# Kernel optimization log

Hardware: AMD Instinct MI355X
Metric: run time of the kernel (lower is better)

The kernel has to match this reference:

```python
import jax, jax.numpy as jnp
import numpy as np

N = 4096  # seq len, used for cos/sin positional reweighting


def _non_neg(x):
    # exp(x) for x<0, x+1 for x>=0
    return jnp.where(x < 0, jnp.exp(x), x + 1.0)


def setup_inputs() -> dict:
    key = jax.random.key(0)
    kq, kk, kv = jax.random.split(key, 3)
    shape = (4, 16, N, 64)
    q = jax.random.normal(kq, shape, dtype=jnp.float32)
    k = jax.random.normal(kk, shape, dtype=jnp.float32)
    v = jax.random.normal(kv, shape, dtype=jnp.float32)
    return {"q": q, "k": k, "v": v}


def reference(q, k, v):
    s = q.shape[-2]
    pos = (jnp.pi / 2.0 / s) * jnp.arange(s, dtype=q.dtype)
    cos = jnp.cos(pos)[:, None]  # [S, 1], broadcasts over feature dim
    sin = jnp.sin(pos)[:, None]
    qf = _non_neg(q)
    kf = _non_neg(k)
    q_cos, q_sin = qf * cos, qf * sin  # [B, H, S, D]
    k_cos, k_sin = kf * cos, kf * sin
    # O(N) kv aggregation: [B, H, D, Dv]
    kv_cos = jnp.einsum('bhsd,bhse->bhde', k_cos, v)
    kv_sin = jnp.einsum('bhsd,bhse->bhde', k_sin, v)
    out = jnp.einsum('bhsd,bhde->bhse', q_cos, kv_cos) + \
          jnp.einsum('bhsd,bhde->bhse', q_sin, kv_sin)
    return out
```

## Files before the change

### kernel.cpp

```cpp
#include <hip/hip_runtime.h>
#include <math.h>

#define SLEN 4096
#define DH   64
#define BHN  64
#define CH   16
#define ROWSPER 256

typedef float  f32x4   __attribute__((ext_vector_type(4)));
typedef float  f32x16  __attribute__((ext_vector_type(16)));
typedef short  s16x4   __attribute__((ext_vector_type(4)));
typedef __bf16 bf16x8  __attribute__((ext_vector_type(8)));

static constexpr float ANG = 3.8349519697141029e-4f;

static __device__ __forceinline__ float featf(float x) {
    return x < 0.f ? __expf(x) : x + 1.f;
}
static __device__ __forceinline__ float b2f(short s) {
    unsigned u = ((unsigned)(unsigned short)s) << 16;
    float f; __builtin_memcpy(&f, &u, 4); return f;
}
static __device__ __forceinline__ short f2b(float f) {
    __bf16 h = (__bf16)f; short s; __builtin_memcpy(&s, &h, 2); return s;
}

__global__ __launch_bounds__(256) void kv_partial(const float* __restrict__ k,
                                                  const float* __restrict__ v,
                                                  short* __restrict__ part)
{
    static constexpr float CJ[8] = {
        1.0f, 0.999999926470f, 0.9999997058633f, 0.9999993381923f,
        0.9999988234532f, 0.9999981616455f, 0.9999973527695f, 0.9999963968250f};
    static constexpr float SJ[8] = {
        0.0f, 3.83495188e-4f, 7.66990319e-4f, 1.15048534e-3f,
        1.53398019e-3f, 1.91747481e-3f, 2.30096915e-3f, 2.68446316e-3f};
    static constexpr float RC16 = 0.99998117528260111f;
    static constexpr float RS16 = 6.1358846491544753e-3f;

    const int bx = blockIdx.x;
    const int bh = bx >> 4, ch = bx & 15;
    const size_t base = (size_t)bh * SLEN * DH;
    const int t  = threadIdx.x;
    const int w  = t >> 6;
    const int l  = t & 63;
    const int m  = l & 31;
    const int g  = l >> 5;
    const int dh = w >> 1;
    const int eh = w & 1;
    const int dcol = dh * 32 + m;
    const int ecol = eh * 32 + m;
    const int s_base = ch * ROWSPER;

    float c0, s0;
    __sincosf(ANG * (float)(s_base + g * 8), &s0, &c0);

    f32x16 accC = {}; f32x16 accS = {};
    float kr[2][8], vr[2][8];

#define LOADS(BUF, STEP) {                                                     \
        const size_t r0 = base + (size_t)(s_base + (STEP) * 16 + g * 8) * DH;  \
        _Pragma("unroll")                                                      \
        for (int j = 0; j < 8; ++j) {                                          \
            kr[BUF][j] = k[r0 + (size_t)j * DH + dcol];                        \
            vr[BUF][j] = v[r0 + (size_t)j * DH + ecol];                        \
        } }

    LOADS(0, 0)
    #pragma unroll
    for (int step = 0; step < 16; ++step) {
        const int buf = step & 1;
        if (step + 1 < 16) LOADS(buf ^ 1, step + 1)
        union { bf16x8 v; __bf16 e[8]; } Ac, As, Bv;
        #pragma unroll
        for (int j = 0; j < 8; ++j) {
            const float kf = featf(kr[buf][j]);
            const float p  = kf * c0;
            const float q  = kf * s0;
            Ac.e[j] = (__bf16)(p * CJ[j] - q * SJ[j]);
            As.e[j] = (__bf16)(q * CJ[j] + p * SJ[j]);
            Bv.e[j] = (__bf16)vr[buf][j];
        }
        accC = __builtin_amdgcn_mfma_f32_32x32x16_bf16(Ac.v, Bv.v, accC, 0, 0, 0);
        accS = __builtin_amdgcn_mfma_f32_32x32x16_bf16(As.v, Bv.v, accS, 0, 0, 0);
        const float cn = c0 * RC16 - s0 * RS16;
        s0 = s0 * RC16 + c0 * RS16;
        c0 = cn;
    }
#undef LOADS

    const size_t pb = (size_t)bx * 8192;
    #pragma unroll
    for (int r = 0; r < 16; ++r) {
        const int drow = dh * 32 + (r & 3) + 8 * (r >> 2) + 4 * g;
        const size_t o = pb + (size_t)drow * 64 + ecol;
        part[o]        = f2b(accC[r]);
        part[o + 4096] = f2b(accS[r]);
    }
}

__global__ __launch_bounds__(256) void kv_reduce(const short* __restrict__ part,
                                                 short* __restrict__ kvT)
{
    const int bx = blockIdx.x;
    const int bh = bx >> 3, seg = bx & 7;
    const size_t pbase = (size_t)bh * CH * 8192;
    const int j0 = seg * 1024 + threadIdx.x * 4;
    float acc[4] = {};
    #pragma unroll
    for (int c = 0; c < CH; ++c) {
        const s16x4 sv = *(const s16x4*)&part[pbase + (size_t)c * 8192 + j0];
        #pragma unroll
        for (int i = 0; i < 4; ++i) acc[i] += b2f(sv[i]);
    }
    const int cs = j0 >> 12;
    const int d  = (j0 >> 6) & 63;
    const int e0 = j0 & 63;
    #pragma unroll
    for (int i = 0; i < 4; ++i)
        kvT[(size_t)bh * 8192 + cs * 4096 + (e0 + i) * 64 + d] = f2b(acc[i]);
}

__global__ __launch_bounds__(256) void out_kernel(const float* __restrict__ q,
                                                  const short* __restrict__ kvT,
                                                  float* __restrict__ out)
{
    const int bx = blockIdx.x;
    const int bh = bx >> 4, chunk = bx & 15;
    const int t = threadIdx.x;
    const int wv = t >> 6, ln = t & 63, m = ln & 15, g = ln >> 4;
    const size_t qbase = (size_t)bh * SLEN * DH;
    const size_t kvb   = (size_t)bh * 8192;

    bf16x8 Bc[4][2], Bs[4][2];
    #pragma unroll
    for (int nt = 0; nt < 4; ++nt)
        #pragma unroll
        for (int b = 0; b < 2; ++b) {
            const int off = (nt * 16 + m) * 64 + b * 32 + g * 8;
            Bc[nt][b] = *(const bf16x8*)&kvT[kvb + off];
            Bs[nt][b] = *(const bf16x8*)&kvT[kvb + 4096 + off];
        }

    const int sA = chunk * 256 + wv * 16 + m;
    f32x4 qb[4], qn[4];
    #pragma unroll
    for (int p = 0; p < 4; ++p)
        qb[p] = *(const f32x4*)&q[qbase + (size_t)sA * DH + (p >> 1) * 32 + g * 8 + (p & 1) * 4];

    for (int it = 0; it < 4; ++it) {
        const int srow = sA + it * 64;
        if (it < 3) {
            #pragma unroll
            for (int p = 0; p < 4; ++p)
                qn[p] = *(const f32x4*)&q[qbase + (size_t)(srow + 64) * DH + (p >> 1) * 32 + g * 8 + (p & 1) * 4];
        }
        float sn, c;
        __sincosf(ANG * (float)srow, &sn, &c);
        union { bf16x8 v; __bf16 e[8]; } Ac[2], As[2];
        #pragma unroll
        for (int p = 0; p < 4; ++p) {
            #pragma unroll
            for (int i = 0; i < 4; ++i) {
                const float qf = featf(qb[p][i]);
                Ac[p >> 1].e[(p & 1) * 4 + i] = (__bf16)(qf * c);
                As[p >> 1].e[(p & 1) * 4 + i] = (__bf16)(qf * sn);
            }
        }
        f32x4 acc[4] = {};
        #pragma unroll
        for (int nt = 0; nt < 4; ++nt) {
            acc[nt] = __builtin_amdgcn_mfma_f32_16x16x32_bf16(Ac[0].v, Bc[nt][0], acc[nt], 0, 0, 0);
            acc[nt] = __builtin_amdgcn_mfma_f32_16x16x32_bf16(Ac[1].v, Bc[nt][1], acc[nt], 0, 0, 0);
            acc[nt] = __builtin_amdgcn_mfma_f32_16x16x32_bf16(As[0].v, Bs[nt][0], acc[nt], 0, 0, 0);
            acc[nt] = __builtin_amdgcn_mfma_f32_16x16x32_bf16(As[1].v, Bs[nt][1], acc[nt], 0, 0, 0);
        }
        const int s0 = chunk * 256 + (it * 4 + wv) * 16;
        #pragma unroll
        for (int r = 0; r < 4; ++r) {
            const size_t ob = ((size_t)bh * SLEN + s0 + g * 4 + r) * 64;
            #pragma unroll
            for (int nt = 0; nt < 4; ++nt)
                out[ob + nt * 16 + m] = acc[nt][r];
        }
        if (it < 3) {
            #pragma unroll
            for (int p = 0; p < 4; ++p) qb[p] = qn[p];
        }
    }
}

extern "C" void kernel_launch(void* const* d_in, const int* in_sizes, int n_in,
                              void* d_out, int out_size, void* d_ws, size_t ws_size,
                              hipStream_t stream) {
    const float* q = (const float*)d_in[0];
    const float* k = (const float*)d_in[1];
    const float* v = (const float*)d_in[2];
    float* out  = (float*)d_out;
    short* part = (short*)d_ws;
    short* kvT  = (short*)((char*)d_ws + (size_t)BHN * CH * 8192 * 2);

    hipLaunchKernelGGL(kv_partial, dim3(BHN * CH), dim3(256), 0, stream, k, v, part);
    hipLaunchKernelGGL(kv_reduce,  dim3(BHN * 8),  dim3(256), 0, stream, part, kvT);
    hipLaunchKernelGGL(out_kernel, dim3(BHN * 16), dim3(256), 0, stream, q, kvT, out);
}
```

Before: 66.32 us.

## Restructure kv_partial into single-wave block with async global-to-LDS triple buffering

kv_partial shrinks from four waves to one wave per block, and that wave now computes all four 32x32 output quadrants. K and V tiles are streamed into LDS with global_load_lds in a three-buffer pipeline guarded by vmcnt waits. This replaces strided per-lane scalar global loads with coalesced 16-byte DMA, and each wave reuses its k features across two V halves. The cost is a quarter of the threads in flight per block, more accumulator registers (eight 16-wide accumulators) and a longer serial loop per wave, so latency hiding now depends on the software pipeline.

```diff
diff --git a/kernel.cpp b/kernel.cpp
--- a/kernel.cpp
+++ b/kernel.cpp
@@ -25,9 +25,13 @@
     __bf16 h = (__bf16)f; short s; __builtin_memcpy(&s, &h, 2); return s;
 }
 
-__global__ __launch_bounds__(256) void kv_partial(const float* __restrict__ k,
-                                                  const float* __restrict__ v,
-                                                  short* __restrict__ part)
+#define GLD(SRC, DST) __builtin_amdgcn_global_load_lds(                        \
+    (const __attribute__((address_space(1))) void*)(SRC),                      \
+    (__attribute__((address_space(3))) void*)(DST), 16, 0, 0)
+
+__global__ __launch_bounds__(64) void kv_partial(const float* __restrict__ k,
+                                                 const float* __restrict__ v,
+                                                 short* __restrict__ part)
 {
     static constexpr float CJ[8] = {
         1.0f, 0.999999926470f, 0.9999997058633f, 0.9999993381923f,
@@ -38,64 +42,97 @@
     static constexpr float RC16 = 0.99998117528260111f;
     static constexpr float RS16 = 6.1358846491544753e-3f;
 
+    __shared__ float kbuf[3][16][64];
+    __shared__ float vbuf[3][16][64];
+
     const int bx = blockIdx.x;
     const int bh = bx >> 4, ch = bx & 15;
     const size_t base = (size_t)bh * SLEN * DH;
-    const int t  = threadIdx.x;
-    const int w  = t >> 6;
-    const int l  = t & 63;
-    const int m  = l & 31;
-    const int g  = l >> 5;
-    const int dh = w >> 1;
-    const int eh = w & 1;
-    const int dcol = dh * 32 + m;
-    const int ecol = eh * 32 + m;
+    const int l = threadIdx.x;
+    const int m = l & 31;
+    const int g = l >> 5;
     const int s_base = ch * ROWSPER;
 
     float c0, s0;
     __sincosf(ANG * (float)(s_base + g * 8), &s0, &c0);
 
-    f32x16 accC = {}; f32x16 accS = {};
-    float kr[2][8], vr[2][8];
-
-#define LOADS(BUF, STEP) {                                                     \
-        const size_t r0 = base + (size_t)(s_base + (STEP) * 16 + g * 8) * DH;  \
+    f32x16 aC00 = {}, aC01 = {}, aC10 = {}, aC11 = {};
+    f32x16 aS00 = {}, aS01 = {}, aS10 = {}, aS11 = {};
+
+#define STAGE(TILE, BUF) do {                                                  \
+        const float* gk_ = k + base + (size_t)(s_base + (TILE) * 16) * DH + l * 4; \
+        const float* gv_ = v + base + (size_t)(s_base + (TILE) * 16) * DH + l * 4; \
         _Pragma("unroll")                                                      \
-        for (int j = 0; j < 8; ++j) {                                          \
-            kr[BUF][j] = k[r0 + (size_t)j * DH + dcol];                        \
-            vr[BUF][j] = v[r0 + (size_t)j * DH + ecol];                        \
-        } }
-
-    LOADS(0, 0)
-    #pragma unroll
-    for (int step = 0; step < 16; ++step) {
-        const int buf = step & 1;
-        if (step + 1 < 16) LOADS(buf ^ 1, step + 1)
-        union { bf16x8 v; __bf16 e[8]; } Ac, As, Bv;
+        for (int i_ = 0; i_ < 4; ++i_) {                                       \
+            GLD(gk_ + i_ * 256, &kbuf[BUF][i_ * 4][0]);                        \
+            GLD(gv_ + i_ * 256, &vbuf[BUF][i_ * 4][0]);                        \
+        } } while (0)
+
+    STAGE(0, 0);
+    STAGE(1, 1);
+
+    #pragma unroll
+    for (int t = 0; t < 16; ++t) {
+        const int buf = t % 3;
+        if (t == 15) { asm volatile("s_waitcnt vmcnt(0)" ::: "memory"); }
+        else         { asm volatile("s_waitcnt vmcnt(8)" ::: "memory"); }
+        __builtin_amdgcn_sched_barrier(0);
+
+        float k0[8], k1[8], v0[8], v1[8];
         #pragma unroll
         for (int j = 0; j < 8; ++j) {
-            const float kf = featf(kr[buf][j]);
-            const float p  = kf * c0;
-            const float q  = kf * s0;
-            Ac.e[j] = (__bf16)(p * CJ[j] - q * SJ[j]);
-            As.e[j] = (__bf16)(q * CJ[j] + p * SJ[j]);
-            Bv.e[j] = (__bf16)vr[buf][j];
-        }
-        accC = __builtin_amdgcn_mfma_f32_32x32x16_bf16(Ac.v, Bv.v, accC, 0, 0, 0);
-        accS = __builtin_amdgcn_mfma_f32_32x32x16_bf16(As.v, Bv.v, accS, 0, 0, 0);
+            k0[j] = kbuf[buf][g * 8 + j][m];
+            k1[j] = kbuf[buf][g * 8 + j][32 + m];
+            v0[j] = vbuf[buf][g * 8 + j][m];
+            v1[j] = vbuf[buf][g * 8 + j][32 + m];
+        }
+        __builtin_amdgcn_sched_barrier(0);
+        if (t + 2 < 16) STAGE(t + 2, (t + 2) % 3);
+        __builtin_amdgcn_sched_barrier(0);
+
+        union { bf16x8 v; __bf16 e[8]; } Ac0, Ac1, As0, As1, B0, B1;
+        #pragma unroll
+        for (int j = 0; j < 8; ++j) {
+            const float cj = c0 * CJ[j] - s0 * SJ[j];
+            const float sj = s0 * CJ[j] + c0 * SJ[j];
+            const float f0 = featf(k0[j]);
+            const float f1 = featf(k1[j]);
+            Ac0.e[j] = (__bf16)(f0 * cj);
+            As0.e[j] = (__bf16)(f0 * sj);
+            Ac1.e[j] = (__bf16)(f1 * cj);
+            As1.e[j] = (__bf16)(f1 * sj);
+            B0.e[j]  = (__bf16)v0[j];
+            B1.e[j]  = (__bf16)v1[j];
+        }
+        aC00 = __builtin_amdgcn_mfma_f32_32x32x16_bf16(Ac0.v, B0.v, aC00, 0, 0, 0);
+        aC01 = __builtin_amdgcn_mfma_f32_32x32x16_bf16(Ac0.v, B1.v, aC01, 0, 0, 0);
+        aC10 = __builtin_amdgcn_mfma_f32_32x32x16_bf16(Ac1.v, B0.v, aC10, 0, 0, 0);
+        aC11 = __builtin_amdgcn_mfma_f32_32x32x16_bf16(Ac1.v, B1.v, aC11, 0, 0, 0);
+        aS00 = __builtin_amdgcn_mfma_f32_32x32x16_bf16(As0.v, B0.v, aS00, 0, 0, 0);
+        aS01 = __builtin_amdgcn_mfma_f32_32x32x16_bf16(As0.v, B1.v, aS01, 0, 0, 0);
+        aS10 = __builtin_amdgcn_mfma_f32_32x32x16_bf16(As1.v, B0.v, aS10, 0, 0, 0);
+        aS11 = __builtin_amdgcn_mfma_f32_32x32x16_bf16(As1.v, B1.v, aS11, 0, 0, 0);
+
         const float cn = c0 * RC16 - s0 * RS16;
         s0 = s0 * RC16 + c0 * RS16;
         c0 = cn;
     }
-#undef LOADS
+#undef STAGE
 
     const size_t pb = (size_t)bx * 8192;
     #pragma unroll
     for (int r = 0; r < 16; ++r) {
-        const int drow = dh * 32 + (r & 3) + 8 * (r >> 2) + 4 * g;
-        const size_t o = pb + (size_t)drow * 64 + ecol;
-        part[o]        = f2b(accC[r]);
-        part[o + 4096] = f2b(accS[r]);
+        const int rb = (r & 3) + 8 * (r >> 2) + 4 * g;
+        const size_t o0 = pb + (size_t)rb * 64;
+        const size_t o1 = pb + (size_t)(32 + rb) * 64;
+        part[o0 + m]             = f2b(aC00[r]);
+        part[o0 + 32 + m]        = f2b(aC01[r]);
+        part[o1 + m]             = f2b(aC10[r]);
+        part[o1 + 32 + m]        = f2b(aC11[r]);
+        part[o0 + 4096 + m]      = f2b(aS00[r]);
+        part[o0 + 4096 + 32 + m] = f2b(aS01[r]);
+        part[o1 + 4096 + m]      = f2b(aS10[r]);
+        part[o1 + 4096 + 32 + m] = f2b(aS11[r]);
     }
 }
 
@@ -200,7 +237,7 @@
     short* part = (short*)d_ws;
     short* kvT  = (short*)((char*)d_ws + (size_t)BHN * CH * 8192 * 2);
 
-    hipLaunchKernelGGL(kv_partial, dim3(BHN * CH), dim3(256), 0, stream, k, v, part);
+    hipLaunchKernelGGL(kv_partial, dim3(BHN * CH), dim3(64),  0, stream, k, v, part);
     hipLaunchKernelGGL(kv_reduce,  dim3(BHN * 8),  dim3(256), 0, stream, part, kvT);
     hipLaunchKernelGGL(out_kernel, dim3(BHN * 16), dim3(256), 0, stream, q, kvT, out);
 }
```

Measured after the change: 69.18 us. 1.04x slower.

## Stage K/V tiles through LDS with async global_load_lds in a 4-deep pipeline

Applied to the files above, without the earlier changes.

The kv_partial kernel now loads each 16-row K/V tile with global_load_lds (16-byte direct-to-LDS loads) into a 4-slot shared ring, keeping three tiles in flight. Manual vmcnt waits and barriers order the stages. Threads then read their strided columns from LDS instead of issuing many scalar global loads, which is meant to improve coalescing and latency hiding. The price is extra LDS traffic, a block barrier every step, and sensitivity to the hand-counted vmcnt values. The rotation math was also reordered so the angle is computed per row before multiplying by the feature.

```diff
diff --git a/kernel.cpp b/kernel.cpp
--- a/kernel.cpp
+++ b/kernel.cpp
@@ -24,6 +24,10 @@
 static __device__ __forceinline__ short f2b(float f) {
     __bf16 h = (__bf16)f; short s; __builtin_memcpy(&s, &h, 2); return s;
 }
+
+#define GLD(SRC, DST) __builtin_amdgcn_global_load_lds(                        \
+    (const __attribute__((address_space(1))) void*)(SRC),                      \
+    (__attribute__((address_space(3))) void*)(DST), 16, 0, 0)
 
 __global__ __launch_bounds__(256) void kv_partial(const float* __restrict__ k,
                                                   const float* __restrict__ v,
@@ -38,62 +42,78 @@
     static constexpr float RC16 = 0.99998117528260111f;
     static constexpr float RS16 = 6.1358846491544753e-3f;
 
+    __shared__ float kbuf[4][16][64];
+    __shared__ float vbuf[4][16][64];
+
     const int bx = blockIdx.x;
     const int bh = bx >> 4, ch = bx & 15;
     const size_t base = (size_t)bh * SLEN * DH;
-    const int t  = threadIdx.x;
-    const int w  = t >> 6;
-    const int l  = t & 63;
+    const int tid = threadIdx.x;
+    const int w  = tid >> 6;
+    const int l  = tid & 63;
     const int m  = l & 31;
     const int g  = l >> 5;
     const int dh = w >> 1;
     const int eh = w & 1;
-    const int dcol = dh * 32 + m;
-    const int ecol = eh * 32 + m;
     const int s_base = ch * ROWSPER;
 
     float c0, s0;
     __sincosf(ANG * (float)(s_base + g * 8), &s0, &c0);
 
     f32x16 accC = {}; f32x16 accS = {};
-    float kr[2][8], vr[2][8];
-
-#define LOADS(BUF, STEP) {                                                     \
-        const size_t r0 = base + (size_t)(s_base + (STEP) * 16 + g * 8) * DH;  \
+
+#define STAGE(TILE, BUF) do {                                                  \
+        const size_t r_ = base + (size_t)(s_base + (TILE) * 16 + w * 4) * DH + l * 4; \
+        GLD(k + r_, &kbuf[BUF][w * 4][0]);                                     \
+        GLD(v + r_, &vbuf[BUF][w * 4][0]);                                     \
+    } while (0)
+
+#define VMW(N) asm volatile("s_waitcnt vmcnt(" #N ")" ::: "memory")
+
+#define STEP(T, NW) do {                                                       \
+        VMW(NW);                                  \
+        __builtin_amdgcn_s_barrier();        \
+        __builtin_amdgcn_sched_barrier(0);    \
+        if ((T) + 3 < 16) STAGE((T) + 3, ((T) + 3) & 3);                       \
+        const int buf_ = (T) & 3;                                              \
+        float kf_[8], vf_[8];                                                  \
         _Pragma("unroll")                                                      \
         for (int j = 0; j < 8; ++j) {                                          \
-            kr[BUF][j] = k[r0 + (size_t)j * DH + dcol];                        \
-            vr[BUF][j] = v[r0 + (size_t)j * DH + ecol];                        \
-        } }
-
-    LOADS(0, 0)
-    #pragma unroll
-    for (int step = 0; step < 16; ++step) {
-        const int buf = step & 1;
-        if (step + 1 < 16) LOADS(buf ^ 1, step + 1)
-        union { bf16x8 v; __bf16 e[8]; } Ac, As, Bv;
-        #pragma unroll
-        for (int j = 0; j < 8; ++j) {
-            const float kf = featf(kr[buf][j]);
-            const float p  = kf * c0;
-            const float q  = kf * s0;
-            Ac.e[j] = (__bf16)(p * CJ[j] - q * SJ[j]);
-            As.e[j] = (__bf16)(q * CJ[j] + p * SJ[j]);
-            Bv.e[j] = (__bf16)vr[buf][j];
-        }
-        accC = __builtin_amdgcn_mfma_f32_32x32x16_bf16(Ac.v, Bv.v, accC, 0, 0, 0);
-        accS = __builtin_amdgcn_mfma_f32_32x32x16_bf16(As.v, Bv.v, accS, 0, 0, 0);
-        const float cn = c0 * RC16 - s0 * RS16;
-        s0 = s0 * RC16 + c0 * RS16;
-        c0 = cn;
-    }
-#undef LOADS
+            kf_[j] = kbuf[buf_][g * 8 + j][dh * 32 + m];                       \
+            vf_[j] = vbuf[buf_][g * 8 + j][eh * 32 + m];                       \
+        }                                                                      \
+        union { bf16x8 vv; __bf16 e[8]; } Ac_, As_, Bv_;                       \
+        _Pragma("unroll")                                                      \
+        for (int j = 0; j < 8; ++j) {                                          \
+            const float cj_ = c0 * CJ[j] - s0 * SJ[j];                         \
+            const float sj_ = s0 * CJ[j] + c0 * SJ[j];                         \
+            const float f_  = featf(kf_[j]);                                   \
+            Ac_.e[j] = (__bf16)(f_ * cj_);                                     \
+            As_.e[j] = (__bf16)(f_ * sj_);                                     \
+            Bv_.e[j] = (__bf16)vf_[j];                                         \
+        }                                                                      \
+        accC = __builtin_amdgcn_mfma_f32_32x32x16_bf16(Ac_.vv, Bv_.vv, accC, 0, 0, 0); \
+        accS = __builtin_amdgcn_mfma_f32_32x32x16_bf16(As_.vv, Bv_.vv, accS, 0, 0, 0); \
+        { const float cn_ = c0 * RC16 - s0 * RS16;                             \
+          s0 = s0 * RC16 + c0 * RS16; c0 = cn_; }                              \
+    } while (0)
+
+    STAGE(0, 0); STAGE(1, 1); STAGE(2, 2);
+
+    STEP(0, 4);  STEP(1, 4);  STEP(2, 4);  STEP(3, 4);
+    STEP(4, 4);  STEP(5, 4);  STEP(6, 4);  STEP(7, 4);
+    STEP(8, 4);  STEP(9, 4);  STEP(10, 4); STEP(11, 4);
+    STEP(12, 4); STEP(13, 4); STEP(14, 2); STEP(15, 0);
+
+#undef STEP
+#undef VMW
+#undef STAGE
 
     const size_t pb = (size_t)bx * 8192;
     #pragma unroll
     for (int r = 0; r < 16; ++r) {
         const int drow = dh * 32 + (r & 3) + 8 * (r >> 2) + 4 * g;
-        const size_t o = pb + (size_t)drow * 64 + ecol;
+        const size_t o = pb + (size_t)drow * 64 + eh * 32 + m;
         part[o]        = f2b(accC[r]);
         part[o + 4096] = f2b(accS[r]);
     }
```

Result: slower. 69.99 us (+5.5%).

## Stage k/v tiles into LDS with async global_load_lds double buffering

Applied to the files above, without the earlier changes.

In kv_partial, k and v are no longer read by per-thread scalar global loads. Each block now copies 32-row tiles into shared memory with 16-byte global_load_lds transfers, double-buffered and separated by block barriers. Waves then read their columns from LDS, so each element is fetched from global memory once per block instead of once per wave that uses it, and the requests are wider. The cost is a barrier per tile, LDS traffic, and recomputing the per-row rotation angles in the inner loop.

```diff
diff --git a/kernel.cpp b/kernel.cpp
--- a/kernel.cpp
+++ b/kernel.cpp
@@ -6,6 +6,8 @@
 #define BHN  64
 #define CH   16
 #define ROWSPER 256
+#define TROWS 32
+#define NTILES 8
 
 typedef float  f32x4   __attribute__((ext_vector_type(4)));
 typedef float  f32x16  __attribute__((ext_vector_type(16)));
@@ -24,6 +26,10 @@
 static __device__ __forceinline__ short f2b(float f) {
     __bf16 h = (__bf16)f; short s; __builtin_memcpy(&s, &h, 2); return s;
 }
+
+#define GLD(SRC, DST) __builtin_amdgcn_global_load_lds(                        \
+    (const __attribute__((address_space(1))) void*)(SRC),                      \
+    (__attribute__((address_space(3))) void*)(DST), 16, 0, 0)
 
 __global__ __launch_bounds__(256) void kv_partial(const float* __restrict__ k,
                                                   const float* __restrict__ v,
@@ -38,62 +44,76 @@
     static constexpr float RC16 = 0.99998117528260111f;
     static constexpr float RS16 = 6.1358846491544753e-3f;
 
+    __shared__ float kbuf[2][TROWS][64];
+    __shared__ float vbuf[2][TROWS][64];
+
     const int bx = blockIdx.x;
     const int bh = bx >> 4, ch = bx & 15;
     const size_t base = (size_t)bh * SLEN * DH;
-    const int t  = threadIdx.x;
-    const int w  = t >> 6;
-    const int l  = t & 63;
+    const int tid = threadIdx.x;
+    const int w  = tid >> 6;
+    const int l  = tid & 63;
     const int m  = l & 31;
     const int g  = l >> 5;
     const int dh = w >> 1;
     const int eh = w & 1;
-    const int dcol = dh * 32 + m;
-    const int ecol = eh * 32 + m;
     const int s_base = ch * ROWSPER;
 
     float c0, s0;
     __sincosf(ANG * (float)(s_base + g * 8), &s0, &c0);
 
     f32x16 accC = {}; f32x16 accS = {};
-    float kr[2][8], vr[2][8];
-
-#define LOADS(BUF, STEP) {                                                     \
-        const size_t r0 = base + (size_t)(s_base + (STEP) * 16 + g * 8) * DH;  \
+
+#define STAGE(TILE, BUF) do {                                                  \
         _Pragma("unroll")                                                      \
-        for (int j = 0; j < 8; ++j) {                                          \
-            kr[BUF][j] = k[r0 + (size_t)j * DH + dcol];                        \
-            vr[BUF][j] = v[r0 + (size_t)j * DH + ecol];                        \
-        } }
-
-    LOADS(0, 0)
-    #pragma unroll
-    for (int step = 0; step < 16; ++step) {
-        const int buf = step & 1;
-        if (step + 1 < 16) LOADS(buf ^ 1, step + 1)
-        union { bf16x8 v; __bf16 e[8]; } Ac, As, Bv;
-        #pragma unroll
-        for (int j = 0; j < 8; ++j) {
-            const float kf = featf(kr[buf][j]);
-            const float p  = kf * c0;
-            const float q  = kf * s0;
-            Ac.e[j] = (__bf16)(p * CJ[j] - q * SJ[j]);
-            As.e[j] = (__bf16)(q * CJ[j] + p * SJ[j]);
-            Bv.e[j] = (__bf16)vr[buf][j];
-        }
-        accC = __builtin_amdgcn_mfma_f32_32x32x16_bf16(Ac.v, Bv.v, accC, 0, 0, 0);
-        accS = __builtin_amdgcn_mfma_f32_32x32x16_bf16(As.v, Bv.v, accS, 0, 0, 0);
-        const float cn = c0 * RC16 - s0 * RS16;
-        s0 = s0 * RC16 + c0 * RS16;
-        c0 = cn;
-    }
-#undef LOADS
+        for (int i_ = 0; i_ < 2; ++i_) {                                       \
+            const size_t r_ = base +                                           \
+                (size_t)(s_base + (TILE) * TROWS + w * 8 + i_ * 4) * DH + l * 4; \
+            GLD(k + r_, &kbuf[BUF][w * 8 + i_ * 4][0]);                        \
+            GLD(v + r_, &vbuf[BUF][w * 8 + i_ * 4][0]);                        \
+        } } while (0)
+
+    STAGE(0, 0);
+    __syncthreads();
+
+    #pragma unroll
+    for (int t = 0; t < NTILES; ++t) {
+        const int buf = t & 1;
+        if (t + 1 < NTILES) STAGE(t + 1, buf ^ 1);
+
+        #pragma unroll
+        for (int ks = 0; ks < 2; ++ks) {
+            float kf_[8], vf_[8];
+            #pragma unroll
+            for (int j = 0; j < 8; ++j) {
+                const int r = ks * 16 + g * 8 + j;
+                kf_[j] = kbuf[buf][r][dh * 32 + m];
+                vf_[j] = vbuf[buf][r][eh * 32 + m];
+            }
+            union { bf16x8 vv; __bf16 e[8]; } Ac_, As_, Bv_;
+            #pragma unroll
+            for (int j = 0; j < 8; ++j) {
+                const float cj_ = c0 * CJ[j] - s0 * SJ[j];
+                const float sj_ = s0 * CJ[j] + c0 * SJ[j];
+                const float f_  = featf(kf_[j]);
+                Ac_.e[j] = (__bf16)(f_ * cj_);
+                As_.e[j] = (__bf16)(f_ * sj_);
+                Bv_.e[j] = (__bf16)vf_[j];
+            }
+            accC = __builtin_amdgcn_mfma_f32_32x32x16_bf16(Ac_.vv, Bv_.vv, accC, 0, 0, 0);
+            accS = __builtin_amdgcn_mfma_f32_32x32x16_bf16(As_.vv, Bv_.vv, accS, 0, 0, 0);
+            const float cn_ = c0 * RC16 - s0 * RS16;
+            s0 = s0 * RC16 + c0 * RS16; c0 = cn_;
+        }
+        __syncthreads();
+    }
+#undef STAGE
 
     const size_t pb = (size_t)bx * 8192;
     #pragma unroll
     for (int r = 0; r < 16; ++r) {
         const int drow = dh * 32 + (r & 3) + 8 * (r >> 2) + 4 * g;
-        const size_t o = pb + (size_t)drow * 64 + ecol;
+        const size_t o = pb + (size_t)drow * 64 + eh * 32 + m;
         part[o]        = f2b(accC[r]);
         part[o + 4096] = f2b(accS[r]);
     }
```

New measurement: 68.52 us. 3.3% more time.
